# Optimization experiments

Hardware: AMD Instinct MI355X
Metric: run time of the kernel (lower is better)

The kernel has to match this reference:

```python
import jax, jax.numpy as jnp
import numpy as np

D_MODEL = 1024


def setup_inputs() -> dict:
    key = jax.random.key(0)
    k_x, k_qkv, k_proj, k_b = jax.random.split(key, 4)
    b, t, d = 4, 2048, D_MODEL
    scale = 1.0 / np.sqrt(d)
    x = jax.random.normal(k_x, (b, t, d), dtype=jnp.float32)
    # torch Linear(d, 3d, bias=False): weight [3d, d]; we store transposed [d, 3d]
    w_qkv = jax.random.normal(k_qkv, (d, 3 * d), dtype=jnp.float32) * scale
    w_proj = jax.random.normal(k_proj, (d, d), dtype=jnp.float32) * scale
    b_proj = jax.random.normal(k_b, (d,), dtype=jnp.float32) * scale
    return {"x": x, "w_qkv": w_qkv, "w_proj": w_proj, "b_proj": b_proj}


def reference(x, w_qkv, w_proj, b_proj):
    b, t, d = x.shape
    qkv = jnp.einsum("btd,de->bte", x, w_qkv)  # [b, t, 3d]
    q, k, v = jnp.split(qkv, 3, axis=-1)
    att = jnp.einsum("btd,bsd->bts", q, k) / jnp.sqrt(jnp.float32(d))  # [b, t, t]
    causal = jnp.tril(jnp.ones((t, t), dtype=bool))
    att = jnp.where(causal, att, -jnp.inf)
    att = jax.nn.softmax(att, axis=-1)
    out = jnp.einsum("bts,bsd->btd", att, v)
    return jnp.einsum("btd,de->bte", out, w_proj) + b_proj
```

## Files before the change

### kernel.cpp

```cpp
#include <hip/hip_runtime.h>


typedef __bf16 bf16x8_t __attribute__((ext_vector_type(8)));
typedef float  f32x4_t  __attribute__((ext_vector_type(4)));
typedef float  f32x16_t __attribute__((ext_vector_type(16)));
typedef unsigned short u16;

struct alignas(8) u16x4 { u16 x, y, z, w; };

__device__ inline float bf2f(u16 u) {
  union { unsigned u; float f; } c; c.u = ((unsigned)u) << 16; return c.f;
}
__device__ inline u16 f2bf(float f) {
  union { float f; unsigned u; } c; c.f = f;
  unsigned r = c.u + 0x7fffu + ((c.u >> 16) & 1u);
  return (u16)(r >> 16);
}


#define BAR __builtin_amdgcn_s_barrier()
#define SCB __builtin_amdgcn_sched_barrier(0)
#define LGK asm volatile("s_waitcnt lgkmcnt(0)" ::: "memory")

#define STG(pst, base_, ld2, t_, ksh_)                                         \
  { const char* s0_ = (pst) + ((t_) * 64 + (ksh_) * 32) * 2;                   \
    char* d0_ = (base_) + (((t_) & 1) << 15) + ((ksh_) << 14) + ldst;          \
    __builtin_amdgcn_global_load_lds(                                          \
        (const __attribute__((address_space(1))) unsigned int*)s0_,            \
        (__attribute__((address_space(3))) unsigned int*)d0_, 16, 0, 0);       \
    __builtin_amdgcn_global_load_lds(                                          \
        (const __attribute__((address_space(1))) unsigned int*)(s0_ + 128 * (ld2)), \
        (__attribute__((address_space(3))) unsigned int*)(d0_ + 8192), 16, 0, 0); }

#define RD_A(lAb, ks, mh)                                                      \
  a0 = *(const bf16x8_t*)((lAb) + (ks) * 16384 + (mh) * 4096 + 0 * 1024);      \
  a1 = *(const bf16x8_t*)((lAb) + (ks) * 16384 + (mh) * 4096 + 1 * 1024);      \
  a2 = *(const bf16x8_t*)((lAb) + (ks) * 16384 + (mh) * 4096 + 2 * 1024);      \
  a3 = *(const bf16x8_t*)((lAb) + (ks) * 16384 + (mh) * 4096 + 3 * 1024);

#define RD_B(lBb, ks)                                                          \
  b0 = *(const bf16x8_t*)((lBb) + (ks) * 16384 + 0 * 1024);                    \
  b1 = *(const bf16x8_t*)((lBb) + (ks) * 16384 + 1 * 1024);                    \
  b2 = *(const bf16x8_t*)((lBb) + (ks) * 16384 + 2 * 1024);                    \
  b3 = *(const bf16x8_t*)((lBb) + (ks) * 16384 + 3 * 1024);

#define MM(mh)                                                                 \
  acc[(mh)*4+0][0] = __builtin_amdgcn_mfma_f32_16x16x32_bf16(a0, b0, acc[(mh)*4+0][0], 0, 0, 0); \
  acc[(mh)*4+0][1] = __builtin_amdgcn_mfma_f32_16x16x32_bf16(a0, b1, acc[(mh)*4+0][1], 0, 0, 0); \
  acc[(mh)*4+0][2] = __builtin_amdgcn_mfma_f32_16x16x32_bf16(a0, b2, acc[(mh)*4+0][2], 0, 0, 0); \
  acc[(mh)*4+0][3] = __builtin_amdgcn_mfma_f32_16x16x32_bf16(a0, b3, acc[(mh)*4+0][3], 0, 0, 0); \
  acc[(mh)*4+1][0] = __builtin_amdgcn_mfma_f32_16x16x32_bf16(a1, b0, acc[(mh)*4+1][0], 0, 0, 0); \
  acc[(mh)*4+1][1] = __builtin_amdgcn_mfma_f32_16x16x32_bf16(a1, b1, acc[(mh)*4+1][1], 0, 0, 0); \
  acc[(mh)*4+1][2] = __builtin_amdgcn_mfma_f32_16x16x32_bf16(a1, b2, acc[(mh)*4+1][2], 0, 0, 0); \
  acc[(mh)*4+1][3] = __builtin_amdgcn_mfma_f32_16x16x32_bf16(a1, b3, acc[(mh)*4+1][3], 0, 0, 0); \
  acc[(mh)*4+2][0] = __builtin_amdgcn_mfma_f32_16x16x32_bf16(a2, b0, acc[(mh)*4+2][0], 0, 0, 0); \
  acc[(mh)*4+2][1] = __builtin_amdgcn_mfma_f32_16x16x32_bf16(a2, b1, acc[(mh)*4+2][1], 0, 0, 0); \
  acc[(mh)*4+2][2] = __builtin_amdgcn_mfma_f32_16x16x32_bf16(a2, b2, acc[(mh)*4+2][2], 0, 0, 0); \
  acc[(mh)*4+2][3] = __builtin_amdgcn_mfma_f32_16x16x32_bf16(a2, b3, acc[(mh)*4+2][3], 0, 0, 0); \
  acc[(mh)*4+3][0] = __builtin_amdgcn_mfma_f32_16x16x32_bf16(a3, b0, acc[(mh)*4+3][0], 0, 0, 0); \
  acc[(mh)*4+3][1] = __builtin_amdgcn_mfma_f32_16x16x32_bf16(a3, b1, acc[(mh)*4+3][1], 0, 0, 0); \
  acc[(mh)*4+3][2] = __builtin_amdgcn_mfma_f32_16x16x32_bf16(a3, b2, acc[(mh)*4+3][2], 0, 0, 0); \
  acc[(mh)*4+3][3] = __builtin_amdgcn_mfma_f32_16x16x32_bf16(a3, b3, acc[(mh)*4+3][3], 0, 0, 0);

template<int OUTMODE>
__global__ __launch_bounds__(512, 2)
void gemm8p(const u16* __restrict__ A, const u16* __restrict__ B,
            void* __restrict__ Cv, u16* __restrict__ C2,
            const float* __restrict__ bias,
            int K, int lda, int ldb, int ldc)
{
  const int nx  = gridDim.x;
  const int nwg = nx * gridDim.y;
  const int lin = blockIdx.y * nx + blockIdx.x;
  const int cpx = nwg >> 3;
  const int swz = (lin & 7) * cpx + (lin >> 3);
  const int bn0 = (swz % nx) * 256;
  const int bm0 = (swz / nx) * 256;

  __shared__ __align__(16) u16 lds[65536];
  char* const baseA = (char*)lds;
  char* const baseB = (char*)lds + 65536;

  const int tid  = threadIdx.x;
  const int lane = tid & 63;
  const int wv   = tid >> 6;
  const int wrow = ((wv >> 2) & 1) * 128;
  const int wcol = (wv & 3) * 64;
  const int l15  = lane & 15;
  const int rd_pl = l15 * 64 + ((((lane >> 4) ^ (l15 >> 1)) & 3) << 4);

  const int c_src = (tid & 3) ^ ((tid >> 3) & 3);
  const int s_row = tid >> 2;
  const int ldst  = tid * 16;
  const long ldA2 = (long)lda * 2, ldB2 = (long)ldb * 2;
  const char* pAst = (const char*)A + ((long)bm0 + s_row) * ldA2 + c_src * 16;
  const char* pBst = (const char*)B + ((long)bn0 + s_row) * ldB2 + c_src * 16;

  f32x4_t acc[8][4];
#pragma unroll
  for (int i = 0; i < 8; ++i)
#pragma unroll
    for (int j = 0; j < 4; ++j)
      acc[i][j] = (f32x4_t){0.f, 0.f, 0.f, 0.f};

  const int nt = K >> 6;

  STG(pAst, baseA, ldA2, 0, 0);
  STG(pBst, baseB, ldB2, 0, 0);
  STG(pAst, baseA, ldA2, 0, 1);
  STG(pBst, baseB, ldB2, 0, 1);
  if (nt > 1) STG(pAst, baseA, ldA2, 1, 0);
  asm volatile("s_waitcnt vmcnt(6)" ::: "memory");
  BAR; SCB;

  bf16x8_t a0, a1, a2, a3, b0, b1, b2, b3;

  for (int t = 0; t < nt; ++t) {
    const char* lAb = baseA + ((t & 1) << 15) + wrow * 64 + rd_pl;
    const char* lBb = baseB + ((t & 1) << 15) + wcol * 64 + rd_pl;
    const bool st1 = (t + 1 < nt), st2 = (t + 2 < nt);

    RD_B(lBb, 0);
    RD_A(lAb, 0, 0);
    if (st1) STG(pBst, baseB, ldB2, t + 1, 0);
    BAR; LGK; SCB;
    __builtin_amdgcn_s_setprio(1); MM(0); __builtin_amdgcn_s_setprio(0);
    BAR; SCB;

    RD_A(lAb, 0, 1);
    if (st1) STG(pAst, baseA, ldA2, t + 1, 1);
    BAR; LGK; SCB;
    __builtin_amdgcn_s_setprio(1); MM(1); __builtin_amdgcn_s_setprio(0);
    if (st1) { asm volatile("s_waitcnt vmcnt(6)" ::: "memory"); }
    else     { asm volatile("s_waitcnt vmcnt(0)" ::: "memory"); }
    BAR; SCB;

    RD_B(lBb, 1);
    RD_A(lAb, 1, 0);
    if (st1) STG(pBst, baseB, ldB2, t + 1, 1);
    BAR; LGK; SCB;
    __builtin_amdgcn_s_setprio(1); MM(0); __builtin_amdgcn_s_setprio(0);
    BAR; SCB;

    RD_A(lAb, 1, 1);
    if (st2) STG(pAst, baseA, ldA2, t + 2, 0);
    BAR; LGK; SCB;
    __builtin_amdgcn_s_setprio(1); MM(1); __builtin_amdgcn_s_setprio(0);
    if (st1) {
      if (st2) { asm volatile("s_waitcnt vmcnt(6)" ::: "memory"); }
      else     { asm volatile("s_waitcnt vmcnt(4)" ::: "memory"); }
    }
    BAR; SCB;
  }

  const int rb = bm0 + wrow + ((lane >> 4) << 2);

  if (OUTMODE == 2) {
    if (bn0 >= 2048) {
#pragma unroll
      for (int mi = 0; mi < 8; ++mi) {
        const int s0 = rb + mi * 16;
        const int b_ = s0 >> 11;
        const int s_ = s0 & 2047;
#pragma unroll
        for (int ni = 0; ni < 4; ++ni) {
          const int dcol = bn0 - 2048 + wcol + ni * 16 + l15;
          u16x4 o = {f2bf(acc[mi][ni][0]), f2bf(acc[mi][ni][1]),
                     f2bf(acc[mi][ni][2]), f2bf(acc[mi][ni][3])};
          *(u16x4*)&C2[(((long)b_ * 1024 + dcol) << 11) + s_] = o;
        }
      }
    } else {
      u16* Cb16 = (u16*)Cv;
#pragma unroll
      for (int mi = 0; mi < 8; ++mi)
#pragma unroll
        for (int ni = 0; ni < 4; ++ni) {
          const int col = bn0 + wcol + ni * 16 + l15;
#pragma unroll
          for (int r = 0; r < 4; ++r)
            Cb16[(long)(rb + mi * 16 + r) * ldc + col] = f2bf(acc[mi][ni][r]);
        }
    }
    return;
  }

  float* Cf32 = (float*)Cv;
#pragma unroll
  for (int mi = 0; mi < 8; ++mi)
#pragma unroll
    for (int ni = 0; ni < 4; ++ni) {
      const int col = bn0 + wcol + ni * 16 + l15;
      const float bb = bias[col];
#pragma unroll
      for (int r = 0; r < 4; ++r)
        Cf32[(long)(rb + mi * 16 + r) * ldc + col] = acc[mi][ni][r] + bb;
    }
}

template<int OUTMODE, int GRIDMODE>
__global__ __launch_bounds__(256, 4)
void gemm_bt(const u16* __restrict__ A, const u16* __restrict__ B,
             void* __restrict__ Cv, u16* __restrict__ C2,
             const float* __restrict__ bias, float* __restrict__ rs,
             int K, int lda, int ldb, int ldc,
             long sA, long sB, long sC)
{
  int bn0, bm0;
  if (GRIDMODE == 1) {
    const int x = blockIdx.x;
    int r = (int)((sqrtf(8.f * x + 1.f) - 1.f) * 0.5f);
    while ((r + 1) * (r + 2) / 2 <= x) ++r;
    while (r * (r + 1) / 2 > x) --r;
    bm0 = r * 128;
    bn0 = (x - r * (r + 1) / 2) * 128;
  } else if (GRIDMODE == 2) {
    bn0 = blockIdx.x * 128;
    bm0 = ((int)gridDim.y - 1 - (int)blockIdx.y) * 128;
  } else {
    bn0 = blockIdx.x * 128;
    bm0 = blockIdx.y * 128;
  }
  const long bz = blockIdx.z;
  const u16* Ab = A + bz * sA;
  const u16* Bb = B + bz * sB;
  const int Keff = (GRIDMODE == 2) ? min(K, bm0 + 128) : K;

  __shared__ __align__(16) u16 lA[128 * 64];
  __shared__ __align__(16) u16 lB[128 * 64];

  const int tid  = threadIdx.x;
  const int lane = tid & 63;
  const int wv   = tid >> 6;
  const int wm   = (wv >> 1) << 6;
  const int wn   = (wv & 1) << 6;
  const int ml   = lane & 31;
  const int kh   = lane >> 5;
  const int swzl = ml & 7;

  f32x16_t acc[2][2];
#pragma unroll
  for (int i = 0; i < 2; ++i)
#pragma unroll
    for (int j = 0; j < 2; ++j)
#pragma unroll
      for (int r = 0; r < 16; ++r)
        acc[i][j][r] = 0.f;

  const long ldA2 = (long)lda * 2, ldB2 = (long)ldb * 2;
  const int rowA = tid >> 3;
  const int csw  = (tid & 7) ^ (rowA & 7);
  const char* pA = (const char*)(Ab + (long)bm0 * lda) + (long)rowA * ldA2 + (csw << 4);
  const char* pB = (const char*)(Bb + (long)bn0 * ldb) + (long)rowA * ldB2 + (csw << 4);
  const int ldsbo = tid * 16;

  for (int k0 = 0; k0 < Keff; k0 += 64) {
    const long kb = (long)k0 * 2;
#pragma unroll
    for (int r = 0; r < 4; ++r)
      __builtin_amdgcn_global_load_lds(
          (const __attribute__((address_space(1))) unsigned int*)(pA + kb + (long)(r * 32) * ldA2),
          (__attribute__((address_space(3))) unsigned int*)((char*)lA + ldsbo + r * 4096), 16, 0, 0);
#pragma unroll
    for (int r = 0; r < 4; ++r)
      __builtin_amdgcn_global_load_lds(
          (const __attribute__((address_space(1))) unsigned int*)(pB + kb + (long)(r * 32) * ldB2),
          (__attribute__((address_space(3))) unsigned int*)((char*)lB + ldsbo + r * 4096), 16, 0, 0);
    __syncthreads();

#pragma unroll
    for (int s = 0; s < 4; ++s) {
      const int ck = ((s * 2 + kh) ^ swzl) << 3;
      bf16x8_t A0 = *(const bf16x8_t*)&lA[(wm + ml) * 64 + ck];
      bf16x8_t A1 = *(const bf16x8_t*)&lA[(wm + 32 + ml) * 64 + ck];
      bf16x8_t B0 = *(const bf16x8_t*)&lB[(wn + ml) * 64 + ck];
      bf16x8_t B1 = *(const bf16x8_t*)&lB[(wn + 32 + ml) * 64 + ck];
      acc[0][0] = __builtin_amdgcn_mfma_f32_32x32x16_bf16(A0, B0, acc[0][0], 0, 0, 0);
      acc[0][1] = __builtin_amdgcn_mfma_f32_32x32x16_bf16(A0, B1, acc[0][1], 0, 0, 0);
      acc[1][0] = __builtin_amdgcn_mfma_f32_32x32x16_bf16(A1, B0, acc[1][0], 0, 0, 0);
      acc[1][1] = __builtin_amdgcn_mfma_f32_32x32x16_bf16(A1, B1, acc[1][1], 0, 0, 0);
    }
    __syncthreads();
  }

  if (OUTMODE == 3) {
    const float scale = 0.03125f;
    const bool diag = (bm0 == bn0);
    u16* Cb16 = (u16*)Cv + bz * sC;
    float* rsb = rs + bz * 2048;
#pragma unroll
    for (int i = 0; i < 2; ++i) {
#pragma unroll
      for (int reg = 0; reg < 16; ++reg) {
        const int grow = bm0 + wm + i * 32 + (reg & 3) + 8 * (reg >> 2) + kh * 4;
        const int col0 = bn0 + wn + ml;
        float e0 = (diag && col0 > grow)      ? 0.f : __expf(acc[i][0][reg] * scale);
        float e1 = (diag && col0 + 32 > grow) ? 0.f : __expf(acc[i][1][reg] * scale);
        Cb16[(long)grow * ldc + col0]      = f2bf(e0);
        Cb16[(long)grow * ldc + col0 + 32] = f2bf(e1);
        float rsum = e0 + e1;
#pragma unroll
        for (int m = 1; m < 32; m <<= 1) rsum += __shfl_xor(rsum, m);
        if (ml == 0) atomicAdd(&rsb[grow], rsum);
      }
    }
    return;
  }

  if (OUTMODE == 4) {
    float* rsl = (float*)lA;
    if (tid < 128) rsl[tid] = 1.0f / rs[bz * 2048 + bm0 + tid];
    __syncthreads();
    u16* Cb16 = (u16*)Cv + bz * sC;
#pragma unroll
    for (int i = 0; i < 2; ++i)
#pragma unroll
      for (int j = 0; j < 2; ++j)
#pragma unroll
        for (int reg = 0; reg < 16; ++reg) {
          const int rl  = wm + i * 32 + (reg & 3) + 8 * (reg >> 2) + kh * 4;
          const int col = bn0 + wn + j * 32 + ml;
          Cb16[(long)(bm0 + rl) * ldc + col] = f2bf(acc[i][j][reg] * rsl[rl]);
        }
    return;
  }
}

__global__ __launch_bounds__(256)
void cvt_f32_bf16(const float* __restrict__ in, u16* __restrict__ out) {
  const int i = blockIdx.x * 256 + threadIdx.x;
  float4 v = ((const float4*)in)[i];
  u16x4 o = {f2bf(v.x), f2bf(v.y), f2bf(v.z), f2bf(v.w)};
  ((u16x4*)out)[i] = o;
}

__global__ __launch_bounds__(256)
void transpose_weights(const float* __restrict__ wqkv, u16* __restrict__ wqkvT,
                       const float* __restrict__ wproj, u16* __restrict__ wprojT) {
  const bool isq = blockIdx.x < 96;
  const float* in = isq ? wqkv : wproj;
  u16* out        = isq ? wqkvT : wprojT;
  const int C     = isq ? 3072 : 1024;
  const int c0 = (isq ? blockIdx.x : (blockIdx.x - 96)) * 32;
  const int r0 = blockIdx.y * 32;
  __shared__ float t[32][33];
  const int tx = threadIdx.x & 31, ty = threadIdx.x >> 5;
#pragma unroll
  for (int i = 0; i < 32; i += 8)
    t[ty + i][tx] = in[(long)(r0 + ty + i) * C + (c0 + tx)];
  __syncthreads();
#pragma unroll
  for (int i = 0; i < 32; i += 8)
    out[(long)(c0 + ty + i) * 1024 + (r0 + tx)] = f2bf(t[tx][ty + i]);
}

extern "C" void kernel_launch(void* const* d_in, const int* in_sizes, int n_in,
                              void* d_out, int out_size, void* d_ws, size_t ws_size,
                              hipStream_t stream) {
  (void)in_sizes; (void)n_in; (void)out_size; (void)ws_size;
  const float* x      = (const float*)d_in[0];
  const float* w_qkv  = (const float*)d_in[1];
  const float* w_proj = (const float*)d_in[2];
  const float* b_proj = (const float*)d_in[3];
  float* y = (float*)d_out;
  char*  ws = (char*)d_ws;

  u16* xbf    = (u16*)(ws);
  u16* qk     = (u16*)(ws + (16l << 20));
  u16* wqkvT  = (u16*)(ws + (48l << 20));
  u16* wprojT = (u16*)(ws + (54l << 20));
  u16* vT     = (u16*)(ws + (56l << 20));
  u16* E      = (u16*)(ws + (72l << 20));
  float* rsum = (float*)(ws + (104l << 20));
  u16* attn   = xbf;

  hipMemsetAsync(rsum, 0, 4 * 2048 * sizeof(float), stream);
  cvt_f32_bf16<<<8192, 256, 0, stream>>>(x, xbf);
  transpose_weights<<<dim3(128, 32), 256, 0, stream>>>(w_qkv, wqkvT, w_proj, wprojT);
  gemm8p<2><<<dim3(12, 32), 512, 0, stream>>>(
      xbf, wqkvT, qk, vT, nullptr, 1024, 1024, 1024, 2048);
  gemm_bt<3, 1><<<dim3(136, 1, 4), 256, 0, stream>>>(
      qk, qk + 1024, E, nullptr, nullptr, rsum, 1024, 2048, 2048, 2048,
      (long)2048 * 2048, (long)2048 * 2048, (long)2048 * 2048);
  gemm_bt<4, 2><<<dim3(8, 16, 4), 256, 0, stream>>>(
      E, vT, attn, nullptr, nullptr, rsum, 2048, 2048, 2048, 1024,
      (long)2048 * 2048, (long)1024 * 2048, (long)2048 * 1024);
  gemm8p<1><<<dim3(4, 32), 512, 0, stream>>>(
      attn, wprojT, y, nullptr, b_proj, 1024, 1024, 1024, 1024);
}
```

Baseline: 285.4 us.

## Merge gemm8p half-k phases into one and use gemm_bt for output projection

The gemm8p main loop now loads all eight A fragments and four B fragments for each k-slice at once. It issues both next-tile global-to-LDS stages together and runs all 32 MFMAs after one barrier, using partial lgkmcnt waits so the second half of the MFMAs overlaps the remaining LDS reads. This halves the barriers per k-tile at the cost of four more live bf16x8 registers. Separately, the output projection is switched from gemm8p<1> to gemm_bt<1,0> with a new fp32-plus-bias epilogue, giving smaller tiles and more workgroups for this small GEMM.

```diff
diff --git a/kernel.cpp b/kernel.cpp
--- a/kernel.cpp
+++ b/kernel.cpp
@@ -20,7 +20,6 @@
 
 #define BAR __builtin_amdgcn_s_barrier()
 #define SCB __builtin_amdgcn_sched_barrier(0)
-#define LGK asm volatile("s_waitcnt lgkmcnt(0)" ::: "memory")
 
 #define STG(pst, base_, ld2, t_, ksh_)                                         \
   { const char* s0_ = (pst) + ((t_) * 64 + (ksh_) * 32) * 2;                   \
@@ -32,35 +31,25 @@
         (const __attribute__((address_space(1))) unsigned int*)(s0_ + 128 * (ld2)), \
         (__attribute__((address_space(3))) unsigned int*)(d0_ + 8192), 16, 0, 0); }
 
-#define RD_A(lAb, ks, mh)                                                      \
-  a0 = *(const bf16x8_t*)((lAb) + (ks) * 16384 + (mh) * 4096 + 0 * 1024);      \
-  a1 = *(const bf16x8_t*)((lAb) + (ks) * 16384 + (mh) * 4096 + 1 * 1024);      \
-  a2 = *(const bf16x8_t*)((lAb) + (ks) * 16384 + (mh) * 4096 + 2 * 1024);      \
-  a3 = *(const bf16x8_t*)((lAb) + (ks) * 16384 + (mh) * 4096 + 3 * 1024);
-
-#define RD_B(lBb, ks)                                                          \
+#define RD12(lAb, lBb, ks)                                                     \
   b0 = *(const bf16x8_t*)((lBb) + (ks) * 16384 + 0 * 1024);                    \
   b1 = *(const bf16x8_t*)((lBb) + (ks) * 16384 + 1 * 1024);                    \
   b2 = *(const bf16x8_t*)((lBb) + (ks) * 16384 + 2 * 1024);                    \
-  b3 = *(const bf16x8_t*)((lBb) + (ks) * 16384 + 3 * 1024);
-
-#define MM(mh)                                                                 \
-  acc[(mh)*4+0][0] = __builtin_amdgcn_mfma_f32_16x16x32_bf16(a0, b0, acc[(mh)*4+0][0], 0, 0, 0); \
-  acc[(mh)*4+0][1] = __builtin_amdgcn_mfma_f32_16x16x32_bf16(a0, b1, acc[(mh)*4+0][1], 0, 0, 0); \
-  acc[(mh)*4+0][2] = __builtin_amdgcn_mfma_f32_16x16x32_bf16(a0, b2, acc[(mh)*4+0][2], 0, 0, 0); \
-  acc[(mh)*4+0][3] = __builtin_amdgcn_mfma_f32_16x16x32_bf16(a0, b3, acc[(mh)*4+0][3], 0, 0, 0); \
-  acc[(mh)*4+1][0] = __builtin_amdgcn_mfma_f32_16x16x32_bf16(a1, b0, acc[(mh)*4+1][0], 0, 0, 0); \
-  acc[(mh)*4+1][1] = __builtin_amdgcn_mfma_f32_16x16x32_bf16(a1, b1, acc[(mh)*4+1][1], 0, 0, 0); \
-  acc[(mh)*4+1][2] = __builtin_amdgcn_mfma_f32_16x16x32_bf16(a1, b2, acc[(mh)*4+1][2], 0, 0, 0); \
-  acc[(mh)*4+1][3] = __builtin_amdgcn_mfma_f32_16x16x32_bf16(a1, b3, acc[(mh)*4+1][3], 0, 0, 0); \
-  acc[(mh)*4+2][0] = __builtin_amdgcn_mfma_f32_16x16x32_bf16(a2, b0, acc[(mh)*4+2][0], 0, 0, 0); \
-  acc[(mh)*4+2][1] = __builtin_amdgcn_mfma_f32_16x16x32_bf16(a2, b1, acc[(mh)*4+2][1], 0, 0, 0); \
-  acc[(mh)*4+2][2] = __builtin_amdgcn_mfma_f32_16x16x32_bf16(a2, b2, acc[(mh)*4+2][2], 0, 0, 0); \
-  acc[(mh)*4+2][3] = __builtin_amdgcn_mfma_f32_16x16x32_bf16(a2, b3, acc[(mh)*4+2][3], 0, 0, 0); \
-  acc[(mh)*4+3][0] = __builtin_amdgcn_mfma_f32_16x16x32_bf16(a3, b0, acc[(mh)*4+3][0], 0, 0, 0); \
-  acc[(mh)*4+3][1] = __builtin_amdgcn_mfma_f32_16x16x32_bf16(a3, b1, acc[(mh)*4+3][1], 0, 0, 0); \
-  acc[(mh)*4+3][2] = __builtin_amdgcn_mfma_f32_16x16x32_bf16(a3, b2, acc[(mh)*4+3][2], 0, 0, 0); \
-  acc[(mh)*4+3][3] = __builtin_amdgcn_mfma_f32_16x16x32_bf16(a3, b3, acc[(mh)*4+3][3], 0, 0, 0);
+  b3 = *(const bf16x8_t*)((lBb) + (ks) * 16384 + 3 * 1024);                    \
+  a0 = *(const bf16x8_t*)((lAb) + (ks) * 16384 + 0 * 1024);                    \
+  a1 = *(const bf16x8_t*)((lAb) + (ks) * 16384 + 1 * 1024);                    \
+  a2 = *(const bf16x8_t*)((lAb) + (ks) * 16384 + 2 * 1024);                    \
+  a3 = *(const bf16x8_t*)((lAb) + (ks) * 16384 + 3 * 1024);                    \
+  a4 = *(const bf16x8_t*)((lAb) + (ks) * 16384 + 4096 + 0 * 1024);             \
+  a5 = *(const bf16x8_t*)((lAb) + (ks) * 16384 + 4096 + 1 * 1024);             \
+  a6 = *(const bf16x8_t*)((lAb) + (ks) * 16384 + 4096 + 2 * 1024);             \
+  a7 = *(const bf16x8_t*)((lAb) + (ks) * 16384 + 4096 + 3 * 1024);
+
+#define MM4(r, av)                                                             \
+  acc[r][0] = __builtin_amdgcn_mfma_f32_16x16x32_bf16(av, b0, acc[r][0], 0, 0, 0); \
+  acc[r][1] = __builtin_amdgcn_mfma_f32_16x16x32_bf16(av, b1, acc[r][1], 0, 0, 0); \
+  acc[r][2] = __builtin_amdgcn_mfma_f32_16x16x32_bf16(av, b2, acc[r][2], 0, 0, 0); \
+  acc[r][3] = __builtin_amdgcn_mfma_f32_16x16x32_bf16(av, b3, acc[r][3], 0, 0, 0);
 
 template<int OUTMODE>
 __global__ __launch_bounds__(512, 2)
@@ -113,39 +102,37 @@
   asm volatile("s_waitcnt vmcnt(6)" ::: "memory");
   BAR; SCB;
 
-  bf16x8_t a0, a1, a2, a3, b0, b1, b2, b3;
+  bf16x8_t a0, a1, a2, a3, a4, a5, a6, a7, b0, b1, b2, b3;
 
   for (int t = 0; t < nt; ++t) {
     const char* lAb = baseA + ((t & 1) << 15) + wrow * 64 + rd_pl;
     const char* lBb = baseB + ((t & 1) << 15) + wcol * 64 + rd_pl;
     const bool st1 = (t + 1 < nt), st2 = (t + 2 < nt);
 
-    RD_B(lBb, 0);
-    RD_A(lAb, 0, 0);
+    RD12(lAb, lBb, 0);
     if (st1) STG(pBst, baseB, ldB2, t + 1, 0);
-    BAR; LGK; SCB;
-    __builtin_amdgcn_s_setprio(1); MM(0); __builtin_amdgcn_s_setprio(0);
-    BAR; SCB;
-
-    RD_A(lAb, 0, 1);
     if (st1) STG(pAst, baseA, ldA2, t + 1, 1);
-    BAR; LGK; SCB;
-    __builtin_amdgcn_s_setprio(1); MM(1); __builtin_amdgcn_s_setprio(0);
+    SCB; BAR;
+    asm volatile("s_waitcnt lgkmcnt(4)" ::: "memory"); SCB;
+    __builtin_amdgcn_s_setprio(1);
+    MM4(0, a0); MM4(1, a1); MM4(2, a2); MM4(3, a3);
+    asm volatile("s_waitcnt lgkmcnt(0)" ::: "memory"); SCB;
+    MM4(4, a4); MM4(5, a5); MM4(6, a6); MM4(7, a7);
+    __builtin_amdgcn_s_setprio(0);
     if (st1) { asm volatile("s_waitcnt vmcnt(6)" ::: "memory"); }
     else     { asm volatile("s_waitcnt vmcnt(0)" ::: "memory"); }
     BAR; SCB;
 
-    RD_B(lBb, 1);
-    RD_A(lAb, 1, 0);
+    RD12(lAb, lBb, 1);
     if (st1) STG(pBst, baseB, ldB2, t + 1, 1);
-    BAR; LGK; SCB;
-    __builtin_amdgcn_s_setprio(1); MM(0); __builtin_amdgcn_s_setprio(0);
-    BAR; SCB;
-
-    RD_A(lAb, 1, 1);
     if (st2) STG(pAst, baseA, ldA2, t + 2, 0);
-    BAR; LGK; SCB;
-    __builtin_amdgcn_s_setprio(1); MM(1); __builtin_amdgcn_s_setprio(0);
+    SCB; BAR;
+    asm volatile("s_waitcnt lgkmcnt(4)" ::: "memory"); SCB;
+    __builtin_amdgcn_s_setprio(1);
+    MM4(0, a0); MM4(1, a1); MM4(2, a2); MM4(3, a3);
+    asm volatile("s_waitcnt lgkmcnt(0)" ::: "memory"); SCB;
+    MM4(4, a4); MM4(5, a5); MM4(6, a6); MM4(7, a7);
+    __builtin_amdgcn_s_setprio(0);
     if (st1) {
       if (st2) { asm volatile("s_waitcnt vmcnt(6)" ::: "memory"); }
       else     { asm volatile("s_waitcnt vmcnt(4)" ::: "memory"); }
@@ -324,6 +311,18 @@
         }
     return;
   }
+
+  float* Cf32 = (float*)Cv + bz * sC;
+#pragma unroll
+  for (int i = 0; i < 2; ++i)
+#pragma unroll
+    for (int j = 0; j < 2; ++j)
+#pragma unroll
+      for (int reg = 0; reg < 16; ++reg) {
+        const int row = bm0 + wm + i * 32 + (reg & 3) + 8 * (reg >> 2) + kh * 4;
+        const int col = bn0 + wn + j * 32 + ml;
+        Cf32[(long)row * ldc + col] = acc[i][j][reg] + bias[col];
+      }
 }
 
 __global__ __launch_bounds__(256)
@@ -385,6 +384,6 @@
   gemm_bt<4, 2><<<dim3(8, 16, 4), 256, 0, stream>>>(
       E, vT, attn, nullptr, nullptr, rsum, 2048, 2048, 2048, 1024,
       (long)2048 * 2048, (long)1024 * 2048, (long)2048 * 1024);
-  gemm8p<1><<<dim3(4, 32), 512, 0, stream>>>(
-      attn, wprojT, y, nullptr, b_proj, 1024, 1024, 1024, 1024);
-}
+  gemm_bt<1, 0><<<dim3(8, 64, 1), 256, 0, stream>>>(
+      attn, wprojT, y, nullptr, b_proj, nullptr, 1024, 1024, 1024, 1024, 0, 0, 0);
+}
```

After: 280.8 us. Within noise of the previous version (-1.6%).
